# Kernel tuning notes

Hardware: AMD Instinct MI355X
Metric: run time of the kernel (lower is better)

## Reference

```python
import jax, jax.numpy as jnp
import numpy as np

NBOXES = 4096
MAX_BS = 128
NDIM = 3
NPAIRS = 8192
INV4PI = 0.07957747154594767  # 1/(4*pi), 3D Laplace kernel constant


def setup_inputs() -> dict:
    key = jax.random.key(0)
    k1, k2, k3, k4 = jax.random.split(key, 4)
    q_vec = jax.random.normal(k1, (NBOXES, MAX_BS), dtype=jnp.float32)
    XX_list = jax.random.uniform(k2, (NBOXES, MAX_BS, NDIM), dtype=jnp.float32)
    bs_list = jax.random.randint(k3, (NBOXES,), 0, MAX_BS, dtype=jnp.int32)
    uq_boxes = jax.random.randint(k4, (NPAIRS, 2), 0, NBOXES, dtype=jnp.int32)
    return {"q_vec": q_vec, "XX_list": XX_list, "bs_list": bs_list, "uq_boxes": uq_boxes}


def reference(q_vec, XX_list, bs_list, uq_boxes):
    # Batched gather-kernel-matvec-scatter translation (addto_translation with
    # self_bool=False, kappa=0 => 3D Laplace kernel 1/(4*pi*r)).
    nboxes, max_bs = q_vec.shape
    u_boxes = uq_boxes[:, 0]
    q_boxes = uq_boxes[:, 1]

    Xu = XX_list[u_boxes]  # [P, B, 3] gather target points
    Xq = XX_list[q_boxes]  # [P, B, 3] gather source points

    # pairwise squared distances without materializing [P,B,B,3] diffs
    nu = jnp.sum(Xu * Xu, axis=-1)  # [P, B]
    nq = jnp.sum(Xq * Xq, axis=-1)  # [P, B]
    r2 = nu[:, :, None] + nq[:, None, :] - 2.0 * jnp.einsum('pid,pjd->pij', Xu, Xq)
    r2 = jnp.maximum(r2, 0.0)
    nz = r2 > 0.0
    K = jnp.where(nz, INV4PI / jnp.sqrt(jnp.where(nz, r2, 1.0)), 0.0)  # [P, B, B]

    cols = jnp.arange(max_bs, dtype=jnp.int32)
    col_mask = (cols[None, :] < bs_list[q_boxes][:, None]).astype(q_vec.dtype)  # valid src pts
    row_mask = (cols[None, :] < bs_list[u_boxes][:, None]).astype(q_vec.dtype)  # valid trg pts

    qv = q_vec[q_boxes] * col_mask                         # gather + zero_col_bnd
    out = jnp.einsum('pij,pj->pi', K, qv) * row_mask       # batched kernel matvec

    u_vec = jnp.zeros_like(q_vec).at[u_boxes].add(out)     # index_add_ scatter
    return u_vec
```

## Files before the change

kernel.cpp:

```cpp
#include <hip/hip_runtime.h>

#define MAX_BS 128
#define INV4PI 0.07957747154594767f

__global__ __launch_bounds__(128) void fmm_scalar_kernel(
    const float* __restrict__ q_vec,
    const float* __restrict__ XX,
    const int*   __restrict__ bs_list,
    const int2*  __restrict__ uq_boxes,
    float*       __restrict__ out)
{
    const int p = blockIdx.x;
    const int t = threadIdx.x;

    const int2 uq = uq_boxes[p];
    const int u = __builtin_amdgcn_readfirstlane(uq.x);
    const int q = __builtin_amdgcn_readfirstlane(uq.y);
    const int bs_u = bs_list[u];
    const int bs_q = bs_list[q];

    if (t >= bs_u || bs_q == 0) return;

    const float* __restrict__ Xu = XX + (size_t)u * (MAX_BS * 3);
    const float xu = Xu[3 * t + 0];
    const float yu = Xu[3 * t + 1];
    const float zu = Xu[3 * t + 2];

    const float* __restrict__ Xq = XX + (size_t)q * (MAX_BS * 3);
    const float* __restrict__ qv = q_vec + (size_t)q * MAX_BS;

    float acc = 0.0f;
    if (u != q) {
#pragma unroll 8
        for (int j = 0; j < bs_q; ++j) {
            const float sx = Xq[3 * j + 0];
            const float sy = Xq[3 * j + 1];
            const float sz = Xq[3 * j + 2];
            const float w  = qv[j];
            const float dx = xu - sx;
            const float dy = yu - sy;
            const float dz = zu - sz;
            const float r2 = dx * dx + dy * dy + dz * dz;
            acc = fmaf(w, __builtin_amdgcn_rsqf(r2), acc);
        }
    } else {
#pragma unroll 4
        for (int j = 0; j < bs_q; ++j) {
            const float sx = Xq[3 * j + 0];
            const float sy = Xq[3 * j + 1];
            const float sz = Xq[3 * j + 2];
            const float w  = qv[j];
            const float dx = xu - sx;
            const float dy = yu - sy;
            const float dz = zu - sz;
            const float r2 = dx * dx + dy * dy + dz * dz;
            float rinv = __builtin_amdgcn_rsqf(r2);
            rinv = (r2 > 0.0f) ? rinv : 0.0f;
            acc = fmaf(w, rinv, acc);
        }
    }

    atomicAdd(out + (size_t)u * MAX_BS + t, acc * INV4PI);
}

extern "C" void kernel_launch(void* const* d_in, const int* in_sizes, int n_in,
                              void* d_out, int out_size, void* d_ws, size_t ws_size,
                              hipStream_t stream) {
    const float* q_vec    = (const float*)d_in[0];
    const float* XX_list  = (const float*)d_in[1];
    const int*   bs_list  = (const int*)d_in[2];
    const int2*  uq_boxes = (const int2*)d_in[3];
    float* out = (float*)d_out;

    const int npairs = in_sizes[3] / 2;

    hipMemsetAsync(d_out, 0, (size_t)out_size * sizeof(float), stream);

    fmm_scalar_kernel<<<npairs, 128, 0, stream>>>(
        q_vec, XX_list, bs_list, uq_boxes, out);
}
```

Before: 86.38 us.

## Map one pair per wavefront with two target rows per thread

Each 64-lane wave now processes a whole box pair, with each lane computing two target points (t and t+64) when the target box has more than 64 points. Source coordinates and charges are loaded once and reused for both targets, and the number of waves is halved. Templated bodies specialize the one/two-row and self/non-self cases. Large boxes take twice as long per wave, which may worsen load balance.

```diff
diff --git a/kernel.cpp b/kernel.cpp
--- a/kernel.cpp
+++ b/kernel.cpp
@@ -3,15 +3,53 @@
 #define MAX_BS 128
 #define INV4PI 0.07957747154594767f
 
-__global__ __launch_bounds__(128) void fmm_scalar_kernel(
+template<bool TWO, bool SELF>
+__device__ __forceinline__ void body(
+    const float* __restrict__ Xq, const float* __restrict__ qv,
+    const int bs_q,
+    const float xu0, const float yu0, const float zu0,
+    const float xu1, const float yu1, const float zu1,
+    float& acc0, float& acc1)
+{
+#pragma unroll 8
+    for (int j = 0; j < bs_q; ++j) {
+        const float sx = Xq[3 * j + 0];
+        const float sy = Xq[3 * j + 1];
+        const float sz = Xq[3 * j + 2];
+        const float w  = qv[j];
+
+        const float dx0 = xu0 - sx;
+        const float dy0 = yu0 - sy;
+        const float dz0 = zu0 - sz;
+        const float r20 = dx0 * dx0 + dy0 * dy0 + dz0 * dz0;
+        float ri0 = __builtin_amdgcn_rsqf(r20);
+        if (SELF) ri0 = (r20 > 0.0f) ? ri0 : 0.0f;
+        acc0 = fmaf(w, ri0, acc0);
+
+        if (TWO) {
+            const float dx1 = xu1 - sx;
+            const float dy1 = yu1 - sy;
+            const float dz1 = zu1 - sz;
+            const float r21 = dx1 * dx1 + dy1 * dy1 + dz1 * dz1;
+            float ri1 = __builtin_amdgcn_rsqf(r21);
+            if (SELF) ri1 = (r21 > 0.0f) ? ri1 : 0.0f;
+            acc1 = fmaf(w, ri1, acc1);
+        }
+    }
+}
+
+__global__ __launch_bounds__(128) void fmm_wave_kernel(
     const float* __restrict__ q_vec,
     const float* __restrict__ XX,
     const int*   __restrict__ bs_list,
     const int2*  __restrict__ uq_boxes,
-    float*       __restrict__ out)
+    float*       __restrict__ out,
+    const int npairs)
 {
-    const int p = blockIdx.x;
-    const int t = threadIdx.x;
+    const int wv = threadIdx.x >> 6;
+    const int t  = threadIdx.x & 63;
+    const int p  = blockIdx.x * 2 + wv;
+    if (p >= npairs) return;
 
     const int2 uq = uq_boxes[p];
     const int u = __builtin_amdgcn_readfirstlane(uq.x);
@@ -22,45 +60,33 @@
     if (t >= bs_u || bs_q == 0) return;
 
     const float* __restrict__ Xu = XX + (size_t)u * (MAX_BS * 3);
-    const float xu = Xu[3 * t + 0];
-    const float yu = Xu[3 * t + 1];
-    const float zu = Xu[3 * t + 2];
+    const float xu0 = Xu[3 * t + 0];
+    const float yu0 = Xu[3 * t + 1];
+    const float zu0 = Xu[3 * t + 2];
+
+    const bool two = (bs_u > 64);
+    float xu1 = 0.0f, yu1 = 0.0f, zu1 = 0.0f;
+    if (two) {
+        xu1 = Xu[3 * (t + 64) + 0];
+        yu1 = Xu[3 * (t + 64) + 1];
+        zu1 = Xu[3 * (t + 64) + 2];
+    }
 
     const float* __restrict__ Xq = XX + (size_t)q * (MAX_BS * 3);
     const float* __restrict__ qv = q_vec + (size_t)q * MAX_BS;
 
-    float acc = 0.0f;
+    float acc0 = 0.0f, acc1 = 0.0f;
     if (u != q) {
-#pragma unroll 8
-        for (int j = 0; j < bs_q; ++j) {
-            const float sx = Xq[3 * j + 0];
-            const float sy = Xq[3 * j + 1];
-            const float sz = Xq[3 * j + 2];
-            const float w  = qv[j];
-            const float dx = xu - sx;
-            const float dy = yu - sy;
-            const float dz = zu - sz;
-            const float r2 = dx * dx + dy * dy + dz * dz;
-            acc = fmaf(w, __builtin_amdgcn_rsqf(r2), acc);
-        }
+        if (two) body<true , false>(Xq, qv, bs_q, xu0, yu0, zu0, xu1, yu1, zu1, acc0, acc1);
+        else     body<false, false>(Xq, qv, bs_q, xu0, yu0, zu0, xu1, yu1, zu1, acc0, acc1);
     } else {
-#pragma unroll 4
-        for (int j = 0; j < bs_q; ++j) {
-            const float sx = Xq[3 * j + 0];
-            const float sy = Xq[3 * j + 1];
-            const float sz = Xq[3 * j + 2];
-            const float w  = qv[j];
-            const float dx = xu - sx;
-            const float dy = yu - sy;
-            const float dz = zu - sz;
-            const float r2 = dx * dx + dy * dy + dz * dz;
-            float rinv = __builtin_amdgcn_rsqf(r2);
-            rinv = (r2 > 0.0f) ? rinv : 0.0f;
-            acc = fmaf(w, rinv, acc);
-        }
+        if (two) body<true , true >(Xq, qv, bs_q, xu0, yu0, zu0, xu1, yu1, zu1, acc0, acc1);
+        else     body<false, true >(Xq, qv, bs_q, xu0, yu0, zu0, xu1, yu1, zu1, acc0, acc1);
     }
 
-    atomicAdd(out + (size_t)u * MAX_BS + t, acc * INV4PI);
+    float* __restrict__ orow = out + (size_t)u * MAX_BS;
+    atomicAdd(orow + t, acc0 * INV4PI);
+    if (two && (t + 64 < bs_u)) atomicAdd(orow + t + 64, acc1 * INV4PI);
 }
 
 extern "C" void kernel_launch(void* const* d_in, const int* in_sizes, int n_in,
@@ -76,6 +102,7 @@
 
     hipMemsetAsync(d_out, 0, (size_t)out_size * sizeof(float), stream);
 
-    fmm_scalar_kernel<<<npairs, 128, 0, stream>>>(
-        q_vec, XX_list, bs_list, uq_boxes, out);
+    const int nblocks = (npairs + 1) / 2;
+    fmm_wave_kernel<<<nblocks, 128, 0, stream>>>(
+        q_vec, XX_list, bs_list, uq_boxes, out, npairs);
 }
```

Result: no change. 86.91 us (+0.6%).
